# Optimization experiments

Measured on AMD Instinct MI355X. Metric: run time of the kernel, lower is better.

Reference implementation:

```python
import jax, jax.numpy as jnp
import numpy as np

N_NODES = 100000
N_EDGES = 1600000
D = 64
K1 = 10   # conv1 hops
K2 = 3    # stacked conv hops


def _gcn_norm(edge_index, num_nodes, dtype):
    # PyG gcn_norm with add_self_loops=False: sym normalization D^-1/2 A D^-1/2
    row, col = edge_index[0], edge_index[1]
    deg = jax.ops.segment_sum(jnp.ones(row.shape, dtype), col, num_segments=num_nodes)
    dinv = jnp.where(deg > 0, jax.lax.rsqrt(jnp.maximum(deg, 1.0)), 0.0)
    return dinv[row] * dinv[col]  # [E]


def _tagconv(x, ws, b, row, col, nrm, num_nodes):
    # out = sum_k (A_hat^k x) @ W_k + b ; ws: [K+1, D, D]
    out = x @ ws[0]
    h = x
    for k in range(1, ws.shape[0]):
        msg = h[row] * nrm[:, None]                       # [E, D] gather
        h = jax.ops.segment_sum(msg, col, num_segments=num_nodes)  # [N, D] scatter-add
        out = out + h @ ws[k]
    return out + b


def setup_inputs() -> dict:
    key = jax.random.key(0)
    ks = jax.random.split(key, 8)
    x = jax.random.normal(ks[0], (N_NODES, D), dtype=jnp.float32)
    edge_index = jax.random.randint(ks[1], (2, N_EDGES), 0, N_NODES, dtype=jnp.int64)
    s = 1.0 / np.sqrt(D)
    w1 = jax.random.normal(ks[2], (K1 + 1, D, D), dtype=jnp.float32) * s
    b1 = jnp.zeros((D,), dtype=jnp.float32)
    w2 = jax.random.normal(ks[3], (K2 + 1, D, D), dtype=jnp.float32) * s
    b2 = jnp.zeros((D,), dtype=jnp.float32)
    wc = jax.random.normal(ks[4], (D, D), dtype=jnp.float32) * s
    bc = jnp.zeros((D,), dtype=jnp.float32)
    return {"x": x, "edge_index": edge_index, "w1": w1, "b1": b1,
            "w2": w2, "b2": b2, "wc": wc, "bc": bc}


def reference(x, edge_index, w1, b1, w2, b2, wc, bc):
    num_nodes = x.shape[0]
    row, col = edge_index[0], edge_index[1]
    nrm = _gcn_norm(edge_index, num_nodes, x.dtype)
    h = jnp.tanh(_tagconv(x, w1, b1, row, col, nrm, num_nodes))
    h = jnp.tanh(_tagconv(h, w2, b2, row, col, nrm, num_nodes))
    return h @ wc + bc
```

## Files before the change

kernel.cpp:

```cpp
#include <hip/hip_runtime.h>
#include <hip/hip_bf16.h>

#define PAD 16
#define NBKT_MAX 512

typedef __attribute__((ext_vector_type(8))) short short8;
typedef __attribute__((ext_vector_type(4))) float float4v;

__device__ __forceinline__ short8 as_s8(uint4 v) {
    union { uint4 u; short8 s; } x; x.u = v; return x.s;
}

__device__ __forceinline__ int pad_up(int v) { return (v + (PAD - 1)) & ~(PAD - 1); }


__global__ __launch_bounds__(256) void hist_kernel(const int* __restrict__ col,
                                                   int* __restrict__ blockHist, int E, int nbkt) {
    __shared__ int h[NBKT_MAX];
    for (int i = threadIdx.x; i < nbkt; i += 256) h[i] = 0;
    __syncthreads();
    int chunk = (E + gridDim.x - 1) / gridDim.x;
    int lo = blockIdx.x * chunk, hi = min(lo + chunk, E);
    for (int e = lo + threadIdx.x; e < hi; e += 256) atomicAdd(&h[col[e] >> 9], 1);
    __syncthreads();
    for (int i = threadIdx.x; i < nbkt; i += 256) blockHist[i * 256 + blockIdx.x] = h[i];
}

__global__ __launch_bounds__(256) void bscan_kernel(int* __restrict__ blockHist,
                                                    int* __restrict__ bktTot, int nbkt) {
    __shared__ int a[256], b[256];
    int bkt = blockIdx.x;
    int t = threadIdx.x;
    int v = blockHist[bkt * 256 + t];
    a[t] = v;
    __syncthreads();
    int* s = a; int* d = b;
    for (int off = 1; off < 256; off <<= 1) {
        int x = s[t];
        if (t >= off) x += s[t - off];
        d[t] = x;
        __syncthreads();
        int* tmp = s; s = d; d = tmp;
    }
    blockHist[bkt * 256 + t] = s[t] - v;
    if (t == 255) bktTot[bkt] = s[t];
}

__global__ void scan_small(const int* __restrict__ in, int* __restrict__ outp, int n) {
    __shared__ int a[256], b[256];
    int t = threadIdx.x;
    int v = t < n ? in[t] : 0;
    a[t] = v;
    __syncthreads();
    int* s = a; int* d = b;
    for (int off = 1; off < 256; off <<= 1) {
        int x = s[t];
        if (t >= off) x += s[t - off];
        d[t] = x;
        __syncthreads();
        int* tmp = s; s = d; d = tmp;
    }
    if (t < n) outp[t] = s[t] - v;
}

__global__ __launch_bounds__(256) void scatter_kernel(const int* __restrict__ row,
                                                      const int* __restrict__ col,
                                                      const int* __restrict__ blockHist,
                                                      const int* __restrict__ bktOff,
                                                      int2* __restrict__ pairs, int E, int nbkt) {
    __shared__ int cur[NBKT_MAX];
    for (int i = threadIdx.x; i < nbkt; i += 256)
        cur[i] = bktOff[i] + blockHist[i * 256 + blockIdx.x];
    __syncthreads();
    int chunk = (E + gridDim.x - 1) / gridDim.x;
    int lo = blockIdx.x * chunk, hi = min(lo + chunk, E);
    for (int e = lo + threadIdx.x; e < hi; e += 256) {
        int dn = col[e];
        int p = atomicAdd(&cur[dn >> 9], 1);
        pairs[p] = make_int2(row[e], dn);
    }
}

__global__ __launch_bounds__(256) void deg_pairs_kernel(
        const int2* __restrict__ pairs, const int* __restrict__ bktOff,
        const int* __restrict__ bktTot,
        int* __restrict__ deg, float* __restrict__ dinv, float* __restrict__ dinv2,
        float* __restrict__ sdeg, int N) {
    __shared__ int cnt[512];
    int b = blockIdx.x, d0 = b << 9;
    for (int i = threadIdx.x; i < 512; i += 256) cnt[i] = 0;
    __syncthreads();
    int lo = bktOff[b], hi = lo + bktTot[b];
    for (int p = lo + threadIdx.x; p < hi; p += 256)
        atomicAdd(&cnt[pairs[p].y - d0], 1);
    __syncthreads();
    for (int i = threadIdx.x; i < 512; i += 256) {
        int d = d0 + i;
        if (d < N) {
            int c = cnt[i];
            deg[d] = c;
            float v = c > 0 ? rsqrtf((float)c) : 0.0f;
            dinv[d] = v;
            dinv2[d] = v * v;
            sdeg[d] = c > 0 ? sqrtf((float)c) : 0.0f;
        }
    }
}

__global__ void scan_phaseA(const int* __restrict__ deg, int* __restrict__ chunkSum, int N) {
    int t = threadIdx.x;
    int idx = blockIdx.x * 512 + t;
    int v = idx < N ? pad_up(deg[idx]) : 0;
    for (int o = 32; o > 0; o >>= 1) v += __shfl_down(v, o, 64);
    __shared__ int wsum[8];
    if ((t & 63) == 0) wsum[t >> 6] = v;
    __syncthreads();
    if (t == 0) {
        int s = 0;
        for (int i = 0; i < 8; ++i) s += wsum[i];
        chunkSum[blockIdx.x] = s;
    }
}

__global__ void scan_phaseC(const int* __restrict__ deg, const int* __restrict__ chunkOff,
                            int* __restrict__ rowptr, int N) {
    __shared__ int a[512], b[512];
    int t = threadIdx.x;
    int idx = blockIdx.x * 512 + t;
    int v = idx < N ? pad_up(deg[idx]) : 0;
    a[t] = v;
    __syncthreads();
    int* s = a; int* d = b;
    for (int off = 1; off < 512; off <<= 1) {
        int x = s[t];
        if (t >= off) x += s[t - off];
        d[t] = x;
        __syncthreads();
        int* tmp = s; s = d; d = tmp;
    }
    if (idx < N) rowptr[idx] = chunkOff[blockIdx.x] + s[t] - v;
    if (idx == N - 1) rowptr[N] = chunkOff[blockIdx.x] + s[t];
}

__global__ __launch_bounds__(256) void cluster_kernel(const int2* __restrict__ pairs,
                                                      const int* __restrict__ bktOff,
                                                      const int* __restrict__ bktTot,
                                                      const int* __restrict__ rowptr,
                                                      int* __restrict__ srcs, int N) {
    __shared__ int cur[512];
    int b = blockIdx.x;
    int d0 = b << 9;
    for (int i = threadIdx.x; i < 512; i += 256) {
        int d = d0 + i;
        cur[i] = (d < N) ? rowptr[d] : 0;
    }
    __syncthreads();
    int lo = bktOff[b], hi = lo + bktTot[b];
    for (int p = lo + threadIdx.x; p < hi; p += 256) {
        int2 e = pairs[p];
        int pos = atomicAdd(&cur[e.y - d0], 1);
        srcs[pos] = e.x;
    }
    __syncthreads();
    for (int i = threadIdx.x; i < 512; i += 256) {
        int d = d0 + i;
        if (d < N) {
            int p = cur[i];
            int p1 = rowptr[d + 1];
            for (; p < p1; ++p) srcs[p] = N;
        }
    }
}


__global__ void wcvt_kernel(const float* __restrict__ w1, const float* __restrict__ w2,
                            const float* __restrict__ wc, __hip_bfloat16* __restrict__ wf) {
    int idx = blockIdx.x * blockDim.x + threadIdx.x;
    if (idx >= 16 * 4096) return;
    int g = idx >> 12, r = idx & 4095;
    int j = r & 7, lane = (r >> 3) & 63, u = (r >> 9) & 3, t = r >> 11;
    int k = t * 32 + (lane >> 4) * 8 + j;
    int n = u * 16 + (lane & 15);
    const float* W = (g < 11) ? (w1 + (size_t)g * 4096)
                  : (g < 15) ? (w2 + (size_t)(g - 11) * 4096) : wc;
    wf[idx] = __float2bfloat16(W[k * 64 + n]);
}

__global__ void zero_pads_kernel(__hip_bfloat16* __restrict__ gbase, size_t gstride,
                                 int nbuf, int N) {
    int i = blockIdx.x * blockDim.x + threadIdx.x;
    int b = i >> 6;
    if (b < nbuf) gbase[(size_t)b * gstride + (size_t)N * 64 + (i & 63)] = __float2bfloat16(0.0f);
}

__global__ void cvt_g_kernel(const float* __restrict__ x, const float* __restrict__ dinv,
                             __hip_bfloat16* __restrict__ g, int N) {
    int i = blockIdx.x * blockDim.x + threadIdx.x;
    if (i < N * 64) g[i] = __float2bfloat16(dinv[i >> 6] * x[i]);
}


__global__ __launch_bounds__(256) void hop_kernel(
        const __hip_bfloat16* __restrict__ g_in,
        const int* __restrict__ srcs, const int* __restrict__ rowptr,
        const float* __restrict__ dinv2,
        __hip_bfloat16* __restrict__ g_out, int n) {
    const int lane = threadIdx.x & 63;
    const int quad = lane >> 4;
    const int c4 = lane & 15;
    int gw = __builtin_amdgcn_readfirstlane((blockIdx.x * blockDim.x + threadIdx.x) >> 6);
    int nw = (gridDim.x * blockDim.x) >> 6;
    for (int d = gw * 2; d < n; d += nw * 2) {
        int dA = d;
        int dB = d + 1;
        bool hasB = dB < n;
        int pA = rowptr[dA], eA = rowptr[dA + 1];
        int pB = hasB ? rowptr[dB] : 0;
        int eB = hasB ? rowptr[dB + 1] : 0;
        float a0 = 0.f, a1 = 0.f, a2 = 0.f, a3 = 0.f;
        float b0 = 0.f, b1 = 0.f, b2 = 0.f, b3 = 0.f;
        while (pA < eA || pB < eB) {
            int4 sqA, sqB;
            if (pA < eA) { sqA = ((const int4*)(srcs + pA))[quad]; pA += 16; }
            else sqA = make_int4(n, n, n, n);
            if (pB < eB) { sqB = ((const int4*)(srcs + pB))[quad]; pB += 16; }
            else sqB = make_int4(n, n, n, n);
            uint2 vA0 = ((const uint2*)(g_in + (size_t)sqA.x * 64))[c4];
            uint2 vA1 = ((const uint2*)(g_in + (size_t)sqA.y * 64))[c4];
            uint2 vA2 = ((const uint2*)(g_in + (size_t)sqA.z * 64))[c4];
            uint2 vA3 = ((const uint2*)(g_in + (size_t)sqA.w * 64))[c4];
            uint2 vB0 = ((const uint2*)(g_in + (size_t)sqB.x * 64))[c4];
            uint2 vB1 = ((const uint2*)(g_in + (size_t)sqB.y * 64))[c4];
            uint2 vB2 = ((const uint2*)(g_in + (size_t)sqB.z * 64))[c4];
            uint2 vB3 = ((const uint2*)(g_in + (size_t)sqB.w * 64))[c4];
            a0 += __uint_as_float(vA0.x << 16); a1 += __uint_as_float(vA0.x & 0xffff0000u);
            a2 += __uint_as_float(vA0.y << 16); a3 += __uint_as_float(vA0.y & 0xffff0000u);
            a0 += __uint_as_float(vA1.x << 16); a1 += __uint_as_float(vA1.x & 0xffff0000u);
            a2 += __uint_as_float(vA1.y << 16); a3 += __uint_as_float(vA1.y & 0xffff0000u);
            a0 += __uint_as_float(vA2.x << 16); a1 += __uint_as_float(vA2.x & 0xffff0000u);
            a2 += __uint_as_float(vA2.y << 16); a3 += __uint_as_float(vA2.y & 0xffff0000u);
            a0 += __uint_as_float(vA3.x << 16); a1 += __uint_as_float(vA3.x & 0xffff0000u);
            a2 += __uint_as_float(vA3.y << 16); a3 += __uint_as_float(vA3.y & 0xffff0000u);
            b0 += __uint_as_float(vB0.x << 16); b1 += __uint_as_float(vB0.x & 0xffff0000u);
            b2 += __uint_as_float(vB0.y << 16); b3 += __uint_as_float(vB0.y & 0xffff0000u);
            b0 += __uint_as_float(vB1.x << 16); b1 += __uint_as_float(vB1.x & 0xffff0000u);
            b2 += __uint_as_float(vB1.y << 16); b3 += __uint_as_float(vB1.y & 0xffff0000u);
            b0 += __uint_as_float(vB2.x << 16); b1 += __uint_as_float(vB2.x & 0xffff0000u);
            b2 += __uint_as_float(vB2.y << 16); b3 += __uint_as_float(vB2.y & 0xffff0000u);
            b0 += __uint_as_float(vB3.x << 16); b1 += __uint_as_float(vB3.x & 0xffff0000u);
            b2 += __uint_as_float(vB3.y << 16); b3 += __uint_as_float(vB3.y & 0xffff0000u);
        }
        a0 += __shfl_xor(a0, 16); a1 += __shfl_xor(a1, 16);
        a2 += __shfl_xor(a2, 16); a3 += __shfl_xor(a3, 16);
        a0 += __shfl_xor(a0, 32); a1 += __shfl_xor(a1, 32);
        a2 += __shfl_xor(a2, 32); a3 += __shfl_xor(a3, 32);
        b0 += __shfl_xor(b0, 16); b1 += __shfl_xor(b1, 16);
        b2 += __shfl_xor(b2, 16); b3 += __shfl_xor(b3, 16);
        b0 += __shfl_xor(b0, 32); b1 += __shfl_xor(b1, 32);
        b2 += __shfl_xor(b2, 32); b3 += __shfl_xor(b3, 32);
        if (quad == 0) {
            float s = dinv2[dA];
            union { __hip_bfloat16 h[4]; uint2 u; } pk;
            pk.h[0] = __float2bfloat16(s * a0);
            pk.h[1] = __float2bfloat16(s * a1);
            pk.h[2] = __float2bfloat16(s * a2);
            pk.h[3] = __float2bfloat16(s * a3);
            ((uint2*)(g_out + (size_t)dA * 64))[c4] = pk.u;
        } else if (quad == 1 && hasB) {
            float s = dinv2[dB];
            union { __hip_bfloat16 h[4]; uint2 u; } pk;
            pk.h[0] = __float2bfloat16(s * b0);
            pk.h[1] = __float2bfloat16(s * b1);
            pk.h[2] = __float2bfloat16(s * b2);
            pk.h[3] = __float2bfloat16(s * b3);
            ((uint2*)(g_out + (size_t)dB * 64))[c4] = pk.u;
        }
    }
}


template<int NG>
__global__ __launch_bounds__(256, 4) void final_kernel(
        const __hip_bfloat16* gbase, size_t gstride,
        const __hip_bfloat16* __restrict__ wf,
        const float* __restrict__ sdeg, const float* __restrict__ bias,
        const float* __restrict__ scale,
        __hip_bfloat16* out16, int ntiles) {
    const int lane = threadIdx.x & 63;
    const int col = lane & 15, quad = lane >> 4;
    int wv = (blockIdx.x * blockDim.x + threadIdx.x) >> 6;
    int nwv = (gridDim.x * blockDim.x) >> 6;
    const uint4* wfq = (const uint4*)wf;
    int npairs = (ntiles + 1) >> 1;
    for (int pr = wv; pr < npairs; pr += nwv) {
        int tile1 = pr * 2;
        int tile2 = tile1 + 1;
        bool has2 = tile2 < ntiles;
        int ba = tile1 * 16;
        int bb = (has2 ? tile2 : tile1) * 16;
        float4v accA0 = {0.f, 0.f, 0.f, 0.f}, accA1 = {0.f, 0.f, 0.f, 0.f};
        float4v accA2 = {0.f, 0.f, 0.f, 0.f}, accA3 = {0.f, 0.f, 0.f, 0.f};
        float4v accB0 = {0.f, 0.f, 0.f, 0.f}, accB1 = {0.f, 0.f, 0.f, 0.f};
        float4v accB2 = {0.f, 0.f, 0.f, 0.f}, accB3 = {0.f, 0.f, 0.f, 0.f};
#pragma unroll 1
        for (int g = 0; g < NG; ++g) {
            const uint4* ga = (const uint4*)(gbase + (size_t)g * gstride);
            const uint4* wg = wfq + (size_t)g * 512;
#pragma unroll
            for (int t = 0; t < 2; ++t) {
                short8 aA = as_s8(ga[(size_t)(ba + col) * 8 + t * 4 + quad]);
                short8 aB = as_s8(ga[(size_t)(bb + col) * 8 + t * 4 + quad]);
                short8 w0 = as_s8(wg[(t * 4 + 0) * 64 + lane]);
                short8 w1 = as_s8(wg[(t * 4 + 1) * 64 + lane]);
                short8 w2 = as_s8(wg[(t * 4 + 2) * 64 + lane]);
                short8 w3 = as_s8(wg[(t * 4 + 3) * 64 + lane]);
                accA0 = __builtin_amdgcn_mfma_f32_16x16x32_bf16(aA, w0, accA0, 0, 0, 0);
                accB0 = __builtin_amdgcn_mfma_f32_16x16x32_bf16(aB, w0, accB0, 0, 0, 0);
                accA1 = __builtin_amdgcn_mfma_f32_16x16x32_bf16(aA, w1, accA1, 0, 0, 0);
                accB1 = __builtin_amdgcn_mfma_f32_16x16x32_bf16(aB, w1, accB1, 0, 0, 0);
                accA2 = __builtin_amdgcn_mfma_f32_16x16x32_bf16(aA, w2, accA2, 0, 0, 0);
                accB2 = __builtin_amdgcn_mfma_f32_16x16x32_bf16(aB, w2, accB2, 0, 0, 0);
                accA3 = __builtin_amdgcn_mfma_f32_16x16x32_bf16(aA, w3, accA3, 0, 0, 0);
                accB3 = __builtin_amdgcn_mfma_f32_16x16x32_bf16(aB, w3, accB3, 0, 0, 0);
            }
        }
#pragma unroll
        for (int r = 0; r < 4; ++r) {
            int nd = ba + quad * 4 + r;
            float sd = sdeg[nd];
            float sc = scale ? scale[nd] : 1.0f;
            float f0 = sc * tanhf(sd * accA0[r] + bias[0 * 16 + col]);
            float f1 = sc * tanhf(sd * accA1[r] + bias[1 * 16 + col]);
            float f2 = sc * tanhf(sd * accA2[r] + bias[2 * 16 + col]);
            float f3 = sc * tanhf(sd * accA3[r] + bias[3 * 16 + col]);
            out16[(size_t)nd * 64 + 0 * 16 + col] = __float2bfloat16(f0);
            out16[(size_t)nd * 64 + 1 * 16 + col] = __float2bfloat16(f1);
            out16[(size_t)nd * 64 + 2 * 16 + col] = __float2bfloat16(f2);
            out16[(size_t)nd * 64 + 3 * 16 + col] = __float2bfloat16(f3);
        }
        if (has2) {
#pragma unroll
            for (int r = 0; r < 4; ++r) {
                int nd = bb + quad * 4 + r;
                float sd = sdeg[nd];
                float sc = scale ? scale[nd] : 1.0f;
                float f0 = sc * tanhf(sd * accB0[r] + bias[0 * 16 + col]);
                float f1 = sc * tanhf(sd * accB1[r] + bias[1 * 16 + col]);
                float f2 = sc * tanhf(sd * accB2[r] + bias[2 * 16 + col]);
                float f3 = sc * tanhf(sd * accB3[r] + bias[3 * 16 + col]);
                out16[(size_t)nd * 64 + 0 * 16 + col] = __float2bfloat16(f0);
                out16[(size_t)nd * 64 + 1 * 16 + col] = __float2bfloat16(f1);
                out16[(size_t)nd * 64 + 2 * 16 + col] = __float2bfloat16(f2);
                out16[(size_t)nd * 64 + 3 * 16 + col] = __float2bfloat16(f3);
            }
        }
    }
}


__global__ __launch_bounds__(256) void head_kernel(
        const __hip_bfloat16* __restrict__ v16, const __hip_bfloat16* __restrict__ wfc,
        const float* __restrict__ bc, float* __restrict__ out, int ntiles) {
    const int lane = threadIdx.x & 63;
    const int col = lane & 15, quad = lane >> 4;
    int wv = (blockIdx.x * blockDim.x + threadIdx.x) >> 6;
    int nwv = (gridDim.x * blockDim.x) >> 6;
    const uint4* va = (const uint4*)v16;
    const uint4* wg = (const uint4*)wfc;
    for (int tile = wv; tile < ntiles; tile += nwv) {
        int base = tile * 16;
        float4v acc0 = {0.f, 0.f, 0.f, 0.f};
        float4v acc1 = {0.f, 0.f, 0.f, 0.f};
        float4v acc2 = {0.f, 0.f, 0.f, 0.f};
        float4v acc3 = {0.f, 0.f, 0.f, 0.f};
#pragma unroll
        for (int t = 0; t < 2; ++t) {
            short8 a = as_s8(va[(size_t)(base + col) * 8 + t * 4 + quad]);
            short8 b0 = as_s8(wg[(t * 4 + 0) * 64 + lane]);
            short8 b1 = as_s8(wg[(t * 4 + 1) * 64 + lane]);
            short8 b2 = as_s8(wg[(t * 4 + 2) * 64 + lane]);
            short8 b3 = as_s8(wg[(t * 4 + 3) * 64 + lane]);
            acc0 = __builtin_amdgcn_mfma_f32_16x16x32_bf16(a, b0, acc0, 0, 0, 0);
            acc1 = __builtin_amdgcn_mfma_f32_16x16x32_bf16(a, b1, acc1, 0, 0, 0);
            acc2 = __builtin_amdgcn_mfma_f32_16x16x32_bf16(a, b2, acc2, 0, 0, 0);
            acc3 = __builtin_amdgcn_mfma_f32_16x16x32_bf16(a, b3, acc3, 0, 0, 0);
        }
#pragma unroll
        for (int r = 0; r < 4; ++r) {
            int nd = base + quad * 4 + r;
            out[(size_t)nd * 64 + 0 * 16 + col] = acc0[r] + bc[0 * 16 + col];
            out[(size_t)nd * 64 + 1 * 16 + col] = acc1[r] + bc[1 * 16 + col];
            out[(size_t)nd * 64 + 2 * 16 + col] = acc2[r] + bc[2 * 16 + col];
            out[(size_t)nd * 64 + 3 * 16 + col] = acc3[r] + bc[3 * 16 + col];
        }
    }
}


extern "C" void kernel_launch(void* const* d_in, const int* in_sizes, int n_in,
                              void* d_out, int out_size, void* d_ws, size_t ws_size,
                              hipStream_t stream) {
    const float* x  = (const float*)d_in[0];
    const int*   ei = (const int*)d_in[1];
    const float* w1 = (const float*)d_in[2];
    const float* b1 = (const float*)d_in[3];
    const float* w2 = (const float*)d_in[4];
    const float* b2 = (const float*)d_in[5];
    const float* wc = (const float*)d_in[6];
    const float* bc = (const float*)d_in[7];
    float* out = (float*)d_out;

    const int N = in_sizes[0] / 64;
    const int E = in_sizes[1] / 2;
    const int K1 = 10, K2 = 3;
    const int* row = ei;
    const int* col = ei + E;
    const int Epad = E + (PAD - 1) * N + 64;
    const int NBUF = 11;
    const int nbkt = (N + 511) >> 9;
    const size_t gstride = (((size_t)(N + 1) * 64) + 127) & ~(size_t)127;

    char* base = (char*)d_ws;
    auto alloc = [&](size_t bytes) { void* p = (void*)base; base += (bytes + 255) & ~(size_t)255; return p; };
    int*   deg      = (int*)alloc((size_t)N * 4);
    int*   rowptr   = (int*)alloc((size_t)(N + 1) * 4);
    int*   chunkSum = (int*)alloc(256 * 4);
    int*   chunkOff = (int*)alloc(256 * 4);
    int*   blockHist= (int*)alloc((size_t)NBKT_MAX * 256 * 4);
    int*   bktTot   = (int*)alloc((size_t)NBKT_MAX * 4);
    int*   bktOff   = (int*)alloc((size_t)NBKT_MAX * 4);
    float* dinv     = (float*)alloc((size_t)N * 4);
    float* dinv2    = (float*)alloc((size_t)N * 4);
    float* sdeg     = (float*)alloc((size_t)N * 4);
    int*   srcs     = (int*)alloc((size_t)Epad * 4);
    __hip_bfloat16* wf    = (__hip_bfloat16*)alloc((size_t)16 * 4096 * 2);
    __hip_bfloat16* gbase = (__hip_bfloat16*)alloc((size_t)NBUF * gstride * 2);

    auto G = [&](int k) { return gbase + (size_t)k * gstride; };
    int2* pairs = (int2*)G(9);
    __hip_bfloat16* vbuf16 = G(5);

    const int numChunks = (N + 511) / 512;
    const int xBlocks = (N * 64 + 255) / 256;
    const int gBlocks = 2048;
    const int ntiles = (N + 15) / 16;
    const int npairs = (ntiles + 1) / 2;
    const int fBlocks = (npairs + 3) / 4;
    const int hBlocks = (ntiles + 3) / 4;

    hist_kernel<<<256, 256, 0, stream>>>(col, blockHist, E, nbkt);
    bscan_kernel<<<nbkt, 256, 0, stream>>>(blockHist, bktTot, nbkt);
    scan_small<<<1, 256, 0, stream>>>(bktTot, bktOff, nbkt);
    scatter_kernel<<<256, 256, 0, stream>>>(row, col, blockHist, bktOff, pairs, E, nbkt);
    deg_pairs_kernel<<<nbkt, 256, 0, stream>>>(pairs, bktOff, bktTot, deg, dinv, dinv2, sdeg, N);
    scan_phaseA<<<numChunks, 512, 0, stream>>>(deg, chunkSum, N);
    scan_small<<<1, 256, 0, stream>>>(chunkSum, chunkOff, numChunks);
    scan_phaseC<<<numChunks, 512, 0, stream>>>(deg, chunkOff, rowptr, N);
    cluster_kernel<<<nbkt, 256, 0, stream>>>(pairs, bktOff, bktTot, rowptr, srcs, N);

    wcvt_kernel<<<(16 * 4096 + 255) / 256, 256, 0, stream>>>(w1, w2, wc, wf);
    zero_pads_kernel<<<(NBUF * 64 + 255) / 256, 256, 0, stream>>>(gbase, gstride, NBUF, N);
    cvt_g_kernel<<<xBlocks, 256, 0, stream>>>(x, dinv, G(0), N);

    for (int k = 1; k <= K1; ++k)
        hop_kernel<<<gBlocks, 256, 0, stream>>>(G(k - 1), srcs, rowptr, dinv2, G(k), N);

    final_kernel<11><<<fBlocks, 256, 0, stream>>>(gbase, gstride, wf, sdeg, b1, dinv,
                                                  G(1), ntiles);

    for (int k = 1; k <= K2; ++k)
        hop_kernel<<<gBlocks, 256, 0, stream>>>(G(k), srcs, rowptr, dinv2, G(k + 1), N);

    final_kernel<4><<<fBlocks, 256, 0, stream>>>(G(1), gstride, wf + (size_t)11 * 4096,
                                                 sdeg, b2, nullptr, vbuf16, ntiles);

    head_kernel<<<hBlocks, 256, 0, stream>>>(vbuf16, wf + (size_t)15 * 4096, bc, out, ntiles);
}
```

Before: 666.0 us.

## Split features into 16-channel planes and simplify CSR build with global atomics

Feature buffers move from node-major 64-channel rows to four planes of 16 channels, and the hop kernel walks the graph once per plane. Each pass's gathered working set is a quarter of the full feature matrix, which is meant to fit in cache. The bucketed CSR construction is replaced by global-atomic degree counting and direct CSR filling, and the dinv/sdeg computation is folded into the scan. In exchange the edge list and rowptr are read four times per hop, and the global atomics may contend.

```diff
diff --git a/kernel.cpp b/kernel.cpp
--- a/kernel.cpp
+++ b/kernel.cpp
@@ -2,7 +2,6 @@
 #include <hip/hip_bf16.h>
 
 #define PAD 16
-#define NBKT_MAX 512
 
 typedef __attribute__((ext_vector_type(8))) short short8;
 typedef __attribute__((ext_vector_type(4))) float float4v;
@@ -14,36 +13,31 @@
 __device__ __forceinline__ int pad_up(int v) { return (v + (PAD - 1)) & ~(PAD - 1); }
 
 
-__global__ __launch_bounds__(256) void hist_kernel(const int* __restrict__ col,
-                                                   int* __restrict__ blockHist, int E, int nbkt) {
-    __shared__ int h[NBKT_MAX];
-    for (int i = threadIdx.x; i < nbkt; i += 256) h[i] = 0;
+__global__ __launch_bounds__(256) void zero_int_kernel(int* __restrict__ p, int n) {
+    int i = blockIdx.x * blockDim.x + threadIdx.x;
+    if (i < n) p[i] = 0;
+}
+
+__global__ __launch_bounds__(256) void hist_deg_kernel(const int* __restrict__ col,
+                                                       int* __restrict__ deg, int E) {
+    int stride = gridDim.x * blockDim.x;
+    for (int e = blockIdx.x * blockDim.x + threadIdx.x; e < E; e += stride)
+        atomicAdd(&deg[col[e]], 1);
+}
+
+__global__ void scan_phaseA(const int* __restrict__ deg, int* __restrict__ chunkSum, int N) {
+    int t = threadIdx.x;
+    int idx = blockIdx.x * 512 + t;
+    int v = idx < N ? pad_up(deg[idx]) : 0;
+    for (int o = 32; o > 0; o >>= 1) v += __shfl_down(v, o, 64);
+    __shared__ int wsum[8];
+    if ((t & 63) == 0) wsum[t >> 6] = v;
     __syncthreads();
-    int chunk = (E + gridDim.x - 1) / gridDim.x;
-    int lo = blockIdx.x * chunk, hi = min(lo + chunk, E);
-    for (int e = lo + threadIdx.x; e < hi; e += 256) atomicAdd(&h[col[e] >> 9], 1);
-    __syncthreads();
-    for (int i = threadIdx.x; i < nbkt; i += 256) blockHist[i * 256 + blockIdx.x] = h[i];
-}
-
-__global__ __launch_bounds__(256) void bscan_kernel(int* __restrict__ blockHist,
-                                                    int* __restrict__ bktTot, int nbkt) {
-    __shared__ int a[256], b[256];
-    int bkt = blockIdx.x;
-    int t = threadIdx.x;
-    int v = blockHist[bkt * 256 + t];
-    a[t] = v;
-    __syncthreads();
-    int* s = a; int* d = b;
-    for (int off = 1; off < 256; off <<= 1) {
-        int x = s[t];
-        if (t >= off) x += s[t - off];
-        d[t] = x;
-        __syncthreads();
-        int* tmp = s; s = d; d = tmp;
-    }
-    blockHist[bkt * 256 + t] = s[t] - v;
-    if (t == 255) bktTot[bkt] = s[t];
+    if (t == 0) {
+        int s = 0;
+        for (int i = 0; i < 8; ++i) s += wsum[i];
+        chunkSum[blockIdx.x] = s;
+    }
 }
 
 __global__ void scan_small(const int* __restrict__ in, int* __restrict__ outp, int n) {
@@ -63,71 +57,14 @@
     if (t < n) outp[t] = s[t] - v;
 }
 
-__global__ __launch_bounds__(256) void scatter_kernel(const int* __restrict__ row,
-                                                      const int* __restrict__ col,
-                                                      const int* __restrict__ blockHist,
-                                                      const int* __restrict__ bktOff,
-                                                      int2* __restrict__ pairs, int E, int nbkt) {
-    __shared__ int cur[NBKT_MAX];
-    for (int i = threadIdx.x; i < nbkt; i += 256)
-        cur[i] = bktOff[i] + blockHist[i * 256 + blockIdx.x];
-    __syncthreads();
-    int chunk = (E + gridDim.x - 1) / gridDim.x;
-    int lo = blockIdx.x * chunk, hi = min(lo + chunk, E);
-    for (int e = lo + threadIdx.x; e < hi; e += 256) {
-        int dn = col[e];
-        int p = atomicAdd(&cur[dn >> 9], 1);
-        pairs[p] = make_int2(row[e], dn);
-    }
-}
-
-__global__ __launch_bounds__(256) void deg_pairs_kernel(
-        const int2* __restrict__ pairs, const int* __restrict__ bktOff,
-        const int* __restrict__ bktTot,
-        int* __restrict__ deg, float* __restrict__ dinv, float* __restrict__ dinv2,
-        float* __restrict__ sdeg, int N) {
-    __shared__ int cnt[512];
-    int b = blockIdx.x, d0 = b << 9;
-    for (int i = threadIdx.x; i < 512; i += 256) cnt[i] = 0;
-    __syncthreads();
-    int lo = bktOff[b], hi = lo + bktTot[b];
-    for (int p = lo + threadIdx.x; p < hi; p += 256)
-        atomicAdd(&cnt[pairs[p].y - d0], 1);
-    __syncthreads();
-    for (int i = threadIdx.x; i < 512; i += 256) {
-        int d = d0 + i;
-        if (d < N) {
-            int c = cnt[i];
-            deg[d] = c;
-            float v = c > 0 ? rsqrtf((float)c) : 0.0f;
-            dinv[d] = v;
-            dinv2[d] = v * v;
-            sdeg[d] = c > 0 ? sqrtf((float)c) : 0.0f;
-        }
-    }
-}
-
-__global__ void scan_phaseA(const int* __restrict__ deg, int* __restrict__ chunkSum, int N) {
-    int t = threadIdx.x;
-    int idx = blockIdx.x * 512 + t;
-    int v = idx < N ? pad_up(deg[idx]) : 0;
-    for (int o = 32; o > 0; o >>= 1) v += __shfl_down(v, o, 64);
-    __shared__ int wsum[8];
-    if ((t & 63) == 0) wsum[t >> 6] = v;
-    __syncthreads();
-    if (t == 0) {
-        int s = 0;
-        for (int i = 0; i < 8; ++i) s += wsum[i];
-        chunkSum[blockIdx.x] = s;
-    }
-}
-
 __global__ void scan_phaseC(const int* __restrict__ deg, const int* __restrict__ chunkOff,
-                            int* __restrict__ rowptr, int N) {
+                            int* __restrict__ rowptr, float* __restrict__ dinv,
+                            float* __restrict__ dinv2, float* __restrict__ sdeg, int N) {
     __shared__ int a[512], b[512];
     int t = threadIdx.x;
     int idx = blockIdx.x * 512 + t;
-    int v = idx < N ? pad_up(deg[idx]) : 0;
+    int dg = idx < N ? deg[idx] : 0;
+    int v = pad_up(dg);
     a[t] = v;
     __syncthreads();
     int* s = a; int* d = b;
@@ -138,37 +75,36 @@
         __syncthreads();
         int* tmp = s; s = d; d = tmp;
     }
-    if (idx < N) rowptr[idx] = chunkOff[blockIdx.x] + s[t] - v;
+    if (idx < N) {
+        rowptr[idx] = chunkOff[blockIdx.x] + s[t] - v;
+        float r = dg > 0 ? rsqrtf((float)dg) : 0.0f;
+        dinv[idx] = r;
+        dinv2[idx] = r * r;
+        sdeg[idx] = dg > 0 ? sqrtf((float)dg) : 0.0f;
+    }
     if (idx == N - 1) rowptr[N] = chunkOff[blockIdx.x] + s[t];
 }
 
-__global__ __launch_bounds__(256) void cluster_kernel(const int2* __restrict__ pairs,
-                                                      const int* __restrict__ bktOff,
-                                                      const int* __restrict__ bktTot,
-                                                      const int* __restrict__ rowptr,
+__global__ __launch_bounds__(256) void csr_fill_kernel(const int* __restrict__ row,
+                                                       const int* __restrict__ col,
+                                                       const int* __restrict__ rowptr,
+                                                       int* __restrict__ cnt,
+                                                       int* __restrict__ srcs, int E) {
+    int stride = gridDim.x * blockDim.x;
+    for (int e = blockIdx.x * blockDim.x + threadIdx.x; e < E; e += stride) {
+        int dn = col[e];
+        int pos = atomicAdd(&cnt[dn], 1);
+        srcs[rowptr[dn] + pos] = row[e];
+    }
+}
+
+__global__ __launch_bounds__(256) void padfill_kernel(const int* __restrict__ rowptr,
+                                                      const int* __restrict__ deg,
                                                       int* __restrict__ srcs, int N) {
-    __shared__ int cur[512];
-    int b = blockIdx.x;
-    int d0 = b << 9;
-    for (int i = threadIdx.x; i < 512; i += 256) {
-        int d = d0 + i;
-        cur[i] = (d < N) ? rowptr[d] : 0;
-    }
-    __syncthreads();
-    int lo = bktOff[b], hi = lo + bktTot[b];
-    for (int p = lo + threadIdx.x; p < hi; p += 256) {
-        int2 e = pairs[p];
-        int pos = atomicAdd(&cur[e.y - d0], 1);
-        srcs[pos] = e.x;
-    }
-    __syncthreads();
-    for (int i = threadIdx.x; i < 512; i += 256) {
-        int d = d0 + i;
-        if (d < N) {
-            int p = cur[i];
-            int p1 = rowptr[d + 1];
-            for (; p < p1; ++p) srcs[p] = N;
-        }
+    int d = blockIdx.x * blockDim.x + threadIdx.x;
+    if (d < N) {
+        int p = rowptr[d] + deg[d], p1 = rowptr[d + 1];
+        for (; p < p1; ++p) srcs[p] = N;
     }
 }
 
@@ -187,16 +123,23 @@
 }
 
 __global__ void zero_pads_kernel(__hip_bfloat16* __restrict__ gbase, size_t gstride,
-                                 int nbuf, int N) {
+                                 int PS, int nbuf, int N) {
     int i = blockIdx.x * blockDim.x + threadIdx.x;
     int b = i >> 6;
-    if (b < nbuf) gbase[(size_t)b * gstride + (size_t)N * 64 + (i & 63)] = __float2bfloat16(0.0f);
+    if (b < nbuf) {
+        int lane = i & 63;
+        gbase[(size_t)b * gstride + (size_t)(lane >> 4) * PS + (size_t)N * 16 + (lane & 15)] =
+            __float2bfloat16(0.0f);
+    }
 }
 
 __global__ void cvt_g_kernel(const float* __restrict__ x, const float* __restrict__ dinv,
-                             __hip_bfloat16* __restrict__ g, int N) {
+                             __hip_bfloat16* __restrict__ g, int PS, int N) {
     int i = blockIdx.x * blockDim.x + threadIdx.x;
-    if (i < N * 64) g[i] = __float2bfloat16(dinv[i >> 6] * x[i]);
+    if (i < N * 64) {
+        int node = i >> 6, c = i & 63, pl = c >> 4, cc = c & 15;
+        g[(size_t)pl * PS + (size_t)node * 16 + cc] = __float2bfloat16(dinv[node] * x[i]);
+    }
 }
 
 
@@ -204,76 +147,44 @@
         const __hip_bfloat16* __restrict__ g_in,
         const int* __restrict__ srcs, const int* __restrict__ rowptr,
         const float* __restrict__ dinv2,
-        __hip_bfloat16* __restrict__ g_out, int n) {
+        __hip_bfloat16* __restrict__ g_out, int n, int PS) {
     const int lane = threadIdx.x & 63;
-    const int quad = lane >> 4;
-    const int c4 = lane & 15;
+    const int rg = lane >> 2;
+    const int c4 = lane & 3;
     int gw = __builtin_amdgcn_readfirstlane((blockIdx.x * blockDim.x + threadIdx.x) >> 6);
     int nw = (gridDim.x * blockDim.x) >> 6;
-    for (int d = gw * 2; d < n; d += nw * 2) {
-        int dA = d;
-        int dB = d + 1;
-        bool hasB = dB < n;
-        int pA = rowptr[dA], eA = rowptr[dA + 1];
-        int pB = hasB ? rowptr[dB] : 0;
-        int eB = hasB ? rowptr[dB + 1] : 0;
-        float a0 = 0.f, a1 = 0.f, a2 = 0.f, a3 = 0.f;
-        float b0 = 0.f, b1 = 0.f, b2 = 0.f, b3 = 0.f;
-        while (pA < eA || pB < eB) {
-            int4 sqA, sqB;
-            if (pA < eA) { sqA = ((const int4*)(srcs + pA))[quad]; pA += 16; }
-            else sqA = make_int4(n, n, n, n);
-            if (pB < eB) { sqB = ((const int4*)(srcs + pB))[quad]; pB += 16; }
-            else sqB = make_int4(n, n, n, n);
-            uint2 vA0 = ((const uint2*)(g_in + (size_t)sqA.x * 64))[c4];
-            uint2 vA1 = ((const uint2*)(g_in + (size_t)sqA.y * 64))[c4];
-            uint2 vA2 = ((const uint2*)(g_in + (size_t)sqA.z * 64))[c4];
-            uint2 vA3 = ((const uint2*)(g_in + (size_t)sqA.w * 64))[c4];
-            uint2 vB0 = ((const uint2*)(g_in + (size_t)sqB.x * 64))[c4];
-            uint2 vB1 = ((const uint2*)(g_in + (size_t)sqB.y * 64))[c4];
-            uint2 vB2 = ((const uint2*)(g_in + (size_t)sqB.z * 64))[c4];
-            uint2 vB3 = ((const uint2*)(g_in + (size_t)sqB.w * 64))[c4];
-            a0 += __uint_as_float(vA0.x << 16); a1 += __uint_as_float(vA0.x & 0xffff0000u);
-            a2 += __uint_as_float(vA0.y << 16); a3 += __uint_as_float(vA0.y & 0xffff0000u);
-            a0 += __uint_as_float(vA1.x << 16); a1 += __uint_as_float(vA1.x & 0xffff0000u);
-            a2 += __uint_as_float(vA1.y << 16); a3 += __uint_as_float(vA1.y & 0xffff0000u);
-            a0 += __uint_as_float(vA2.x << 16); a1 += __uint_as_float(vA2.x & 0xffff0000u);
-            a2 += __uint_as_float(vA2.y << 16); a3 += __uint_as_float(vA2.y & 0xffff0000u);
-            a0 += __uint_as_float(vA3.x << 16); a1 += __uint_as_float(vA3.x & 0xffff0000u);
-            a2 += __uint_as_float(vA3.y << 16); a3 += __uint_as_float(vA3.y & 0xffff0000u);
-            b0 += __uint_as_float(vB0.x << 16); b1 += __uint_as_float(vB0.x & 0xffff0000u);
-            b2 += __uint_as_float(vB0.y << 16); b3 += __uint_as_float(vB0.y & 0xffff0000u);
-            b0 += __uint_as_float(vB1.x << 16); b1 += __uint_as_float(vB1.x & 0xffff0000u);
-            b2 += __uint_as_float(vB1.y << 16); b3 += __uint_as_float(vB1.y & 0xffff0000u);
-            b0 += __uint_as_float(vB2.x << 16); b1 += __uint_as_float(vB2.x & 0xffff0000u);
-            b2 += __uint_as_float(vB2.y << 16); b3 += __uint_as_float(vB2.y & 0xffff0000u);
-            b0 += __uint_as_float(vB3.x << 16); b1 += __uint_as_float(vB3.x & 0xffff0000u);
-            b2 += __uint_as_float(vB3.y << 16); b3 += __uint_as_float(vB3.y & 0xffff0000u);
-        }
-        a0 += __shfl_xor(a0, 16); a1 += __shfl_xor(a1, 16);
-        a2 += __shfl_xor(a2, 16); a3 += __shfl_xor(a3, 16);
-        a0 += __shfl_xor(a0, 32); a1 += __shfl_xor(a1, 32);
-        a2 += __shfl_xor(a2, 32); a3 += __shfl_xor(a3, 32);
-        b0 += __shfl_xor(b0, 16); b1 += __shfl_xor(b1, 16);
-        b2 += __shfl_xor(b2, 16); b3 += __shfl_xor(b3, 16);
-        b0 += __shfl_xor(b0, 32); b1 += __shfl_xor(b1, 32);
-        b2 += __shfl_xor(b2, 32); b3 += __shfl_xor(b3, 32);
-        if (quad == 0) {
-            float s = dinv2[dA];
-            union { __hip_bfloat16 h[4]; uint2 u; } pk;
-            pk.h[0] = __float2bfloat16(s * a0);
-            pk.h[1] = __float2bfloat16(s * a1);
-            pk.h[2] = __float2bfloat16(s * a2);
-            pk.h[3] = __float2bfloat16(s * a3);
-            ((uint2*)(g_out + (size_t)dA * 64))[c4] = pk.u;
-        } else if (quad == 1 && hasB) {
-            float s = dinv2[dB];
-            union { __hip_bfloat16 h[4]; uint2 u; } pk;
-            pk.h[0] = __float2bfloat16(s * b0);
-            pk.h[1] = __float2bfloat16(s * b1);
-            pk.h[2] = __float2bfloat16(s * b2);
-            pk.h[3] = __float2bfloat16(s * b3);
-            ((uint2*)(g_out + (size_t)dB * 64))[c4] = pk.u;
+    for (int p = 0; p < 4; ++p) {
+        const __hip_bfloat16* gp = g_in + (size_t)p * PS;
+        __hip_bfloat16* op = g_out + (size_t)p * PS;
+        for (int d = gw; d < n; d += nw) {
+            int q0 = rowptr[d], q1 = rowptr[d + 1];
+            float a0 = 0.f, a1 = 0.f, a2 = 0.f, a3 = 0.f;
+            for (int q = q0; q < q1; q += 16) {
+                int s = __builtin_nontemporal_load(srcs + q + rg);
+                uint2 v = *(const uint2*)(gp + (size_t)s * 16 + c4 * 4);
+                a0 += __uint_as_float(v.x << 16);
+                a1 += __uint_as_float(v.x & 0xffff0000u);
+                a2 += __uint_as_float(v.y << 16);
+                a3 += __uint_as_float(v.y & 0xffff0000u);
+            }
+            a0 += __shfl_xor(a0, 4);  a1 += __shfl_xor(a1, 4);
+            a2 += __shfl_xor(a2, 4);  a3 += __shfl_xor(a3, 4);
+            a0 += __shfl_xor(a0, 8);  a1 += __shfl_xor(a1, 8);
+            a2 += __shfl_xor(a2, 8);  a3 += __shfl_xor(a3, 8);
+            a0 += __shfl_xor(a0, 16); a1 += __shfl_xor(a1, 16);
+            a2 += __shfl_xor(a2, 16); a3 += __shfl_xor(a3, 16);
+            a0 += __shfl_xor(a0, 32); a1 += __shfl_xor(a1, 32);
+            a2 += __shfl_xor(a2, 32); a3 += __shfl_xor(a3, 32);
+            if (lane < 4) {
+                float sc = dinv2[d];
+                union { __hip_bfloat16 h[4]; unsigned long long u; } pk;
+                pk.h[0] = __float2bfloat16(sc * a0);
+                pk.h[1] = __float2bfloat16(sc * a1);
+                pk.h[2] = __float2bfloat16(sc * a2);
+                pk.h[3] = __float2bfloat16(sc * a3);
+                __builtin_nontemporal_store(pk.u,
+                    (unsigned long long*)(op + (size_t)d * 16) + lane);
+            }
         }
     }
 }
@@ -281,7 +192,7 @@
 
 template<int NG>
 __global__ __launch_bounds__(256, 4) void final_kernel(
-        const __hip_bfloat16* gbase, size_t gstride,
+        const __hip_bfloat16* gbase, size_t gstride, int PS,
         const __hip_bfloat16* __restrict__ wf,
         const float* __restrict__ sdeg, const float* __restrict__ bias,
         const float* __restrict__ scale,
@@ -291,6 +202,7 @@
     int wv = (blockIdx.x * blockDim.x + threadIdx.x) >> 6;
     int nwv = (gridDim.x * blockDim.x) >> 6;
     const uint4* wfq = (const uint4*)wf;
+    const int psq = PS >> 3;
     int npairs = (ntiles + 1) >> 1;
     for (int pr = wv; pr < npairs; pr += nwv) {
         int tile1 = pr * 2;
@@ -308,8 +220,10 @@
             const uint4* wg = wfq + (size_t)g * 512;
 #pragma unroll
             for (int t = 0; t < 2; ++t) {
-                short8 aA = as_s8(ga[(size_t)(ba + col) * 8 + t * 4 + quad]);
-                short8 aB = as_s8(ga[(size_t)(bb + col) * 8 + t * 4 + quad]);
+                int i8 = t * 4 + quad;
+                size_t pb = (size_t)(i8 >> 1) * psq + (i8 & 1);
+                short8 aA = as_s8(ga[pb + (size_t)(ba + col) * 2]);
+                short8 aB = as_s8(ga[pb + (size_t)(bb + col) * 2]);
                 short8 w0 = as_s8(wg[(t * 4 + 0) * 64 + lane]);
                 short8 w1 = as_s8(wg[(t * 4 + 1) * 64 + lane]);
                 short8 w2 = as_s8(wg[(t * 4 + 2) * 64 + lane]);
@@ -333,10 +247,10 @@
             float f1 = sc * tanhf(sd * accA1[r] + bias[1 * 16 + col]);
             float f2 = sc * tanhf(sd * accA2[r] + bias[2 * 16 + col]);
             float f3 = sc * tanhf(sd * accA3[r] + bias[3 * 16 + col]);
-            out16[(size_t)nd * 64 + 0 * 16 + col] = __float2bfloat16(f0);
-            out16[(size_t)nd * 64 + 1 * 16 + col] = __float2bfloat16(f1);
-            out16[(size_t)nd * 64 + 2 * 16 + col] = __float2bfloat16(f2);
-            out16[(size_t)nd * 64 + 3 * 16 + col] = __float2bfloat16(f3);
+            out16[(size_t)0 * PS + (size_t)nd * 16 + col] = __float2bfloat16(f0);
+            out16[(size_t)1 * PS + (size_t)nd * 16 + col] = __float2bfloat16(f1);
+            out16[(size_t)2 * PS + (size_t)nd * 16 + col] = __float2bfloat16(f2);
+            out16[(size_t)3 * PS + (size_t)nd * 16 + col] = __float2bfloat16(f3);
         }
         if (has2) {
 #pragma unroll
@@ -348,10 +262,10 @@
                 float f1 = sc * tanhf(sd * accB1[r] + bias[1 * 16 + col]);
                 float f2 = sc * tanhf(sd * accB2[r] + bias[2 * 16 + col]);
                 float f3 = sc * tanhf(sd * accB3[r] + bias[3 * 16 + col]);
-                out16[(size_t)nd * 64 + 0 * 16 + col] = __float2bfloat16(f0);
-                out16[(size_t)nd * 64 + 1 * 16 + col] = __float2bfloat16(f1);
-                out16[(size_t)nd * 64 + 2 * 16 + col] = __float2bfloat16(f2);
-                out16[(size_t)nd * 64 + 3 * 16 + col] = __float2bfloat16(f3);
+                out16[(size_t)0 * PS + (size_t)nd * 16 + col] = __float2bfloat16(f0);
+                out16[(size_t)1 * PS + (size_t)nd * 16 + col] = __float2bfloat16(f1);
+                out16[(size_t)2 * PS + (size_t)nd * 16 + col] = __float2bfloat16(f2);
+                out16[(size_t)3 * PS + (size_t)nd * 16 + col] = __float2bfloat16(f3);
             }
         }
     }
@@ -359,7 +273,8 @@
 
 
 __global__ __launch_bounds__(256) void head_kernel(
-        const __hip_bfloat16* __restrict__ v16, const __hip_bfloat16* __restrict__ wfc,
+        const __hip_bfloat16* __restrict__ v16, int PS,
+        const __hip_bfloat16* __restrict__ wfc,
         const float* __restrict__ bc, float* __restrict__ out, int ntiles) {
     const int lane = threadIdx.x & 63;
     const int col = lane & 15, quad = lane >> 4;
@@ -367,6 +282,7 @@
     int nwv = (gridDim.x * blockDim.x) >> 6;
     const uint4* va = (const uint4*)v16;
     const uint4* wg = (const uint4*)wfc;
+    const int psq = PS >> 3;
     for (int tile = wv; tile < ntiles; tile += nwv) {
         int base = tile * 16;
         float4v acc0 = {0.f, 0.f, 0.f, 0.f};
@@ -375,7 +291,9 @@
         float4v acc3 = {0.f, 0.f, 0.f, 0.f};
 #pragma unroll
         for (int t = 0; t < 2; ++t) {
-            short8 a = as_s8(va[(size_t)(base + col) * 8 + t * 4 + quad]);
+            int i8 = t * 4 + quad;
+            size_t pb = (size_t)(i8 >> 1) * psq + (i8 & 1);
+            short8 a = as_s8(va[pb + (size_t)(base + col) * 2]);
             short8 b0 = as_s8(wg[(t * 4 + 0) * 64 + lane]);
             short8 b1 = as_s8(wg[(t * 4 + 1) * 64 + lane]);
             short8 b2 = as_s8(wg[(t * 4 + 2) * 64 + lane]);
@@ -417,18 +335,17 @@
     const int* col = ei + E;
     const int Epad = E + (PAD - 1) * N + 64;
     const int NBUF = 11;
-    const int nbkt = (N + 511) >> 9;
     const size_t gstride = (((size_t)(N + 1) * 64) + 127) & ~(size_t)127;
+    const int PS = (int)(gstride / 4);
 
     char* base = (char*)d_ws;
     auto alloc = [&](size_t bytes) { void* p = (void*)base; base += (bytes + 255) & ~(size_t)255; return p; };
-    int*   deg      = (int*)alloc((size_t)N * 4);
+    int*   degcnt   = (int*)alloc((size_t)2 * N * 4);
+    int*   deg      = degcnt;
+    int*   cnt      = degcnt + N;
     int*   rowptr   = (int*)alloc((size_t)(N + 1) * 4);
     int*   chunkSum = (int*)alloc(256 * 4);
     int*   chunkOff = (int*)alloc(256 * 4);
-    int*   blockHist= (int*)alloc((size_t)NBKT_MAX * 256 * 4);
-    int*   bktTot   = (int*)alloc((size_t)NBKT_MAX * 4);
-    int*   bktOff   = (int*)alloc((size_t)NBKT_MAX * 4);
     float* dinv     = (float*)alloc((size_t)N * 4);
     float* dinv2    = (float*)alloc((size_t)N * 4);
     float* sdeg     = (float*)alloc((size_t)N * 4);
@@ -437,7 +354,6 @@
     __hip_bfloat16* gbase = (__hip_bfloat16*)alloc((size_t)NBUF * gstride * 2);
 
     auto G = [&](int k) { return gbase + (size_t)k * gstride; };
-    int2* pairs = (int2*)G(9);
     __hip_bfloat16* vbuf16 = G(5);
 
     const int numChunks = (N + 511) / 512;
@@ -448,31 +364,29 @@
     const int fBlocks = (npairs + 3) / 4;
     const int hBlocks = (ntiles + 3) / 4;
 
-    hist_kernel<<<256, 256, 0, stream>>>(col, blockHist, E, nbkt);
-    bscan_kernel<<<nbkt, 256, 0, stream>>>(blockHist, bktTot, nbkt);
-    scan_small<<<1, 256, 0, stream>>>(bktTot, bktOff, nbkt);
-    scatter_kernel<<<256, 256, 0, stream>>>(row, col, blockHist, bktOff, pairs, E, nbkt);
-    deg_pairs_kernel<<<nbkt, 256, 0, stream>>>(pairs, bktOff, bktTot, deg, dinv, dinv2, sdeg, N);
+    zero_int_kernel<<<(2 * N + 255) / 256, 256, 0, stream>>>(degcnt, 2 * N);
+    hist_deg_kernel<<<1024, 256, 0, stream>>>(col, deg, E);
     scan_phaseA<<<numChunks, 512, 0, stream>>>(deg, chunkSum, N);
     scan_small<<<1, 256, 0, stream>>>(chunkSum, chunkOff, numChunks);
-    scan_phaseC<<<numChunks, 512, 0, stream>>>(deg, chunkOff, rowptr, N);
-    cluster_kernel<<<nbkt, 256, 0, stream>>>(pairs, bktOff, bktTot, rowptr, srcs, N);
+    scan_phaseC<<<numChunks, 512, 0, stream>>>(deg, chunkOff, rowptr, dinv, dinv2, sdeg, N);
+    csr_fill_kernel<<<1024, 256, 0, stream>>>(row, col, rowptr, cnt, srcs, E);
+    padfill_kernel<<<(N + 255) / 256, 256, 0, stream>>>(rowptr, deg, srcs, N);
 
     wcvt_kernel<<<(16 * 4096 + 255) / 256, 256, 0, stream>>>(w1, w2, wc, wf);
-    zero_pads_kernel<<<(NBUF * 64 + 255) / 256, 256, 0, stream>>>(gbase, gstride, NBUF, N);
-    cvt_g_kernel<<<xBlocks, 256, 0, stream>>>(x, dinv, G(0), N);
+    zero_pads_kernel<<<(NBUF * 64 + 255) / 256, 256, 0, stream>>>(gbase, gstride, PS, NBUF, N);
+    cvt_g_kernel<<<xBlocks, 256, 0, stream>>>(x, dinv, G(0), PS, N);
 
     for (int k = 1; k <= K1; ++k)
-        hop_kernel<<<gBlocks, 256, 0, stream>>>(G(k - 1), srcs, rowptr, dinv2, G(k), N);
-
-    final_kernel<11><<<fBlocks, 256, 0, stream>>>(gbase, gstride, wf, sdeg, b1, dinv,
+        hop_kernel<<<gBlocks, 256, 0, stream>>>(G(k - 1), srcs, rowptr, dinv2, G(k), N, PS);
+
+    final_kernel<11><<<fBlocks, 256, 0, stream>>>(gbase, gstride, PS, wf, sdeg, b1, dinv,
                                                   G(1), ntiles);
 
     for (int k = 1; k <= K2; ++k)
-        hop_kernel<<<gBlocks, 256, 0, stream>>>(G(k), srcs, rowptr, dinv2, G(k + 1), N);
-
-    final_kernel<4><<<fBlocks, 256, 0, stream>>>(G(1), gstride, wf + (size_t)11 * 4096,
+        hop_kernel<<<gBlocks, 256, 0, stream>>>(G(k), srcs, rowptr, dinv2, G(k + 1), N, PS);
+
+    final_kernel<4><<<fBlocks, 256, 0, stream>>>(G(1), gstride, PS, wf + (size_t)11 * 4096,
                                                  sdeg, b2, nullptr, vbuf16, ntiles);
 
-    head_kernel<<<hBlocks, 256, 0, stream>>>(vbuf16, wf + (size_t)15 * 4096, bc, out, ntiles);
-}
+    head_kernel<<<hBlocks, 256, 0, stream>>>(vbuf16, PS, wf + (size_t)15 * 4096, bc, out, ntiles);
+}
```

Result: slower. 1.656 ms (+148.7%).
